# Kernel optimization log

Hardware: AMD Instinct MI355X
Metric: run time of the kernel (lower is better)

## Reference

```python
import jax, jax.numpy as jnp
import numpy as np

B, T = 64, 512
V, E, H, L = 100000, 256, 256, 9


def _lstm(x, Wx, Wh, b):
    # x: [B,T,E] -> hs: [B,T,H]; Keras gate order i,f,c,o
    xg = jnp.einsum('bte,eg->btg', x, Wx) + b  # [B,T,4H]
    h0 = jnp.zeros((x.shape[0], Wh.shape[0]), x.dtype)

    def step(carry, xt):
        h, c = carry
        g = xt + h @ Wh
        i, f, gc, o = jnp.split(g, 4, axis=-1)
        c = jax.nn.sigmoid(f) * c + jax.nn.sigmoid(i) * jnp.tanh(gc)
        h = jax.nn.sigmoid(o) * jnp.tanh(c)
        return (h, c), h

    _, hs = jax.lax.scan(step, (h0, h0), jnp.swapaxes(xg, 0, 1))
    return jnp.swapaxes(hs, 0, 1)


def _crf_log_likelihood(logits, tags, seq_len, trans):
    # logits: [B,T,L], tags: [B,T] int, seq_len: [B] int, trans: [L,L]
    Bb, Tt, Ll = logits.shape
    t_idx = jnp.arange(Tt)
    mask = (t_idx[None, :] < seq_len[:, None]).astype(logits.dtype)  # [B,T]
    # gold path score: unary + pairwise transitions
    unary = jnp.take_along_axis(logits, tags[..., None], axis=-1)[..., 0]  # [B,T]
    unary_score = jnp.sum(unary * mask, axis=-1)
    binary = trans[tags[:, :-1], tags[:, 1:]]  # [B,T-1]
    binary_score = jnp.sum(binary * mask[:, 1:], axis=-1)
    score = unary_score + binary_score
    # forward algorithm (log partition)
    alpha0 = logits[:, 0]  # [B,L]
    step_mask = t_idx[1:, None] < seq_len[None, :]  # [T-1,B]

    def step(alpha, xs):
        logit_t, m = xs  # [B,L], [B]
        new = jax.nn.logsumexp(alpha[:, :, None] + trans[None], axis=1) + logit_t
        alpha = jnp.where(m[:, None], new, alpha)
        return alpha, None

    alpha, _ = jax.lax.scan(step, alpha0, (jnp.swapaxes(logits[:, 1:], 0, 1), step_mask))
    log_norm = jax.nn.logsumexp(alpha, axis=-1)  # [B]
    return score - log_norm


def setup_inputs() -> dict:
    key = jax.random.key(0)
    ks = jax.random.split(key, 12)
    s = 0.05
    return {
        'tokens': jax.random.randint(ks[0], (B, T), 0, V),
        'labels': jax.random.randint(ks[1], (B, T), 0, L),
        'emb_table': jax.random.normal(ks[2], (V, E), jnp.float32) * s,
        'Wx_f': jax.random.normal(ks[3], (E, 4 * H), jnp.float32) * s,
        'Wh_f': jax.random.normal(ks[4], (H, 4 * H), jnp.float32) * s,
        'b_f': jnp.zeros((4 * H,), jnp.float32),
        'Wx_b': jax.random.normal(ks[5], (E, 4 * H), jnp.float32) * s,
        'Wh_b': jax.random.normal(ks[6], (H, 4 * H), jnp.float32) * s,
        'b_b': jnp.zeros((4 * H,), jnp.float32),
        'W_dense': jax.random.normal(ks[7], (2 * H, L), jnp.float32) * s,
        'b_dense': jnp.zeros((L,), jnp.float32),
        'trans': jax.random.uniform(ks[8], (L, L), jnp.float32),
    }


def reference(tokens, labels, emb_table, Wx_f, Wh_f, b_f, Wx_b, Wh_b, b_b, W_dense, b_dense, trans):
    # seq_len = count of non-pad (nonzero) tokens, as in the original call()
    seq_len = jnp.sum((tokens != 0).astype(jnp.int32), axis=-1)  # [B]
    emb = emb_table[tokens]  # [B,T,E]  (dropout inactive at inference)
    h_fwd = _lstm(emb, Wx_f, Wh_f, b_f)
    h_bwd = _lstm(emb[:, ::-1], Wx_b, Wh_b, b_b)[:, ::-1]
    enc = jnp.concatenate([h_fwd, h_bwd], axis=-1)  # [B,T,2H]
    logits = enc @ W_dense + b_dense  # [B,T,L]
    ll = _crf_log_likelihood(logits, labels, seq_len, trans)  # [B]
    return logits, seq_len, ll
```

## Files before the change

### kernel.cpp

```cpp
#include <hip/hip_runtime.h>
#include <hip/hip_fp16.h>


typedef unsigned int  uint32;
typedef unsigned short ushort16;
typedef unsigned long long uint64;
typedef __attribute__((ext_vector_type(8))) short  short8;
typedef __attribute__((ext_vector_type(4))) float  floatx4;
typedef __attribute__((ext_vector_type(2))) _Float16 half2t;

#define BB 64
#define TT 512
#define NT (BB*TT)
#define G4 1024
#define NL 9

__device__ inline float bf2f(ushort16 u) {
  return __builtin_bit_cast(float, ((uint32)u) << 16);
}
__device__ inline ushort16 f2bf(float f) {
  uint32 u = __builtin_bit_cast(uint32, f);
  u += 0x7fffu + ((u >> 16) & 1u);
  return (ushort16)(u >> 16);
}
__device__ inline float sigf(float x)  { return 1.0f / (1.0f + __expf(-x)); }
__device__ inline float tanhf_(float x){ return 1.0f - 2.0f / (1.0f + __expf(2.0f * x)); }

__device__ inline float fdot2_(uint32 w, half2t h, float acc) {
  return __builtin_amdgcn_fdot2(__builtin_bit_cast(half2t, w), h, acc, false);
}

__device__ inline void bar_lds() {
  __builtin_amdgcn_sched_barrier(0);
  asm volatile("s_waitcnt lgkmcnt(0)" ::: "memory");
  __builtin_amdgcn_s_barrier();
  __builtin_amdgcn_sched_barrier(0);
}

__global__ __launch_bounds__(64) void k_seqlen(const int* __restrict__ tokens,
                                               int* __restrict__ slen,
                                               float* __restrict__ out_sl) {
  const int b = blockIdx.x, lane = threadIdx.x;
  int cnt = 0;
  for (int t = lane; t < TT; t += 64) cnt += (tokens[b * TT + t] != 0) ? 1 : 0;
  #pragma unroll
  for (int off = 32; off >= 1; off >>= 1) cnt += __shfl_down(cnt, off, 64);
  if (lane == 0) { slen[b] = cnt; out_sl[b] = (float)cnt; }
}

__global__ __launch_bounds__(256) void k_embed(const int* __restrict__ tokens,
                                               const float* __restrict__ emb,
                                               ushort16* __restrict__ A) {
  const int f = blockIdx.x * 256 + threadIdx.x;
  const int e = f * 4;
  const int row = e >> 8;
  const int col = e & 255;
  const int tok = tokens[row];
  const float4 v = *(const float4*)(emb + (size_t)tok * 256 + col);
  uint32 lo = (uint32)f2bf(v.x) | ((uint32)f2bf(v.y) << 16);
  uint32 hi = (uint32)f2bf(v.z) | ((uint32)f2bf(v.w) << 16);
  *(uint2*)(A + e) = make_uint2(lo, hi);
}

__global__ __launch_bounds__(256) void k_wxprep(const float* __restrict__ Wxf,
                                                const float* __restrict__ Wxb,
                                                ushort16* __restrict__ BT) {
  const int id = blockIdx.x * 256 + threadIdx.x;
  const int c = id >> 8, k = id & 255;
  const float v = (c < G4) ? Wxf[k * G4 + c] : Wxb[k * G4 + (c - G4)];
  BT[c * 256 + k] = f2bf(v);
}

__global__ __launch_bounds__(256) void k_whprep(const float* __restrict__ Wh,
                                                uint32* __restrict__ W2) {
  const int id = blockIdx.x * 256 + threadIdx.x;
  const int k2 = id >> 10, c = id & 1023;
  const float w0 = Wh[(2 * k2) * G4 + c];
  const float w1 = Wh[(2 * k2 + 1) * G4 + c];
  const ushort16 b0 = __builtin_bit_cast(ushort16, (_Float16)w0);
  const ushort16 b1 = __builtin_bit_cast(ushort16, (_Float16)w1);
  W2[id] = ((uint32)b1 << 16) | (uint32)b0;
}

__global__ __launch_bounds__(256) void k_gemm_xg(const ushort16* __restrict__ A,
                                                 const ushort16* __restrict__ BT,
                                                 const float* __restrict__ bias_f,
                                                 const float* __restrict__ bias_b,
                                                 ushort16* __restrict__ xgf,
                                                 ushort16* __restrict__ xgb) {
  __shared__ __align__(16) ushort16 As[64 * 36];
  __shared__ __align__(16) ushort16 Bs[64 * 36];
  const int m0 = blockIdx.x * 64;
  const int n0 = blockIdx.y * 64;
  const int tid = threadIdx.x;
  const int wave = tid >> 6, lane = tid & 63;
  const int lr = tid >> 2;
  const int lc = (tid & 3) * 8;
  const int am = lane & 15, aq = lane >> 4;
  floatx4 acc[4];
  #pragma unroll
  for (int j = 0; j < 4; ++j) acc[j] = (floatx4){0.f, 0.f, 0.f, 0.f};

  for (int k0 = 0; k0 < 256; k0 += 32) {
    const uint4 va = *(const uint4*)(A  + ((m0 + lr) * 256 + k0 + lc));
    const uint4 vb = *(const uint4*)(BT + ((n0 + lr) * 256 + k0 + lc));
    *(uint2*)&As[lr * 36 + lc]     = make_uint2(va.x, va.y);
    *(uint2*)&As[lr * 36 + lc + 4] = make_uint2(va.z, va.w);
    *(uint2*)&Bs[lr * 36 + lc]     = make_uint2(vb.x, vb.y);
    *(uint2*)&Bs[lr * 36 + lc + 4] = make_uint2(vb.z, vb.w);
    __syncthreads();
    union { uint2 u[2]; short8 s; } fa, fb;
    fa.u[0] = *(const uint2*)&As[(wave * 16 + am) * 36 + aq * 8];
    fa.u[1] = *(const uint2*)&As[(wave * 16 + am) * 36 + aq * 8 + 4];
    #pragma unroll
    for (int j = 0; j < 4; ++j) {
      fb.u[0] = *(const uint2*)&Bs[(j * 16 + am) * 36 + aq * 8];
      fb.u[1] = *(const uint2*)&Bs[(j * 16 + am) * 36 + aq * 8 + 4];
      acc[j] = __builtin_amdgcn_mfma_f32_16x16x32_bf16(fa.s, fb.s, acc[j], 0, 0, 0);
    }
    __syncthreads();
  }
  const int orow = m0 + wave * 16 + aq * 4;
  #pragma unroll
  for (int j = 0; j < 4; ++j) {
    const int col = n0 + j * 16 + am;
    const float bv = (col < G4) ? bias_f[col] : bias_b[col - G4];
    #pragma unroll
    for (int r = 0; r < 4; ++r) {
      const float v = acc[j][r] + bv;
      const int row = orow + r;
      if (col < G4) xgf[row * G4 + col] = f2bf(v);
      else          xgb[row * G4 + (col - G4)] = f2bf(v);
    }
  }
}

__global__ __launch_bounds__(256) void k_zero(uint64* __restrict__ xh) {
  xh[blockIdx.x * 256 + threadIdx.x] = 0ull;
}

__global__ __launch_bounds__(512, 2) void k_lstm(const ushort16* __restrict__ xgf,
                                                 const ushort16* __restrict__ xgb,
                                                 const uint32* __restrict__ Whf,
                                                 const uint32* __restrict__ Whb,
                                                 uint64* __restrict__ xh,
                                                 float* __restrict__ enc) {
  __shared__ __align__(16) uint32 h2[2][128];
  __shared__ float gl[512];
  const int bid  = blockIdx.x;
  const int dir  = bid >> 7;
  const int b    = (bid >> 1) & 63;
  const int half = bid & 1;
  const int tid  = threadIdx.x;
  const int l = tid & 63;
  const int q = tid >> 7, r = tid & 127;
  const int col = q * 256 + half * 128 + r;
  const ushort16* __restrict__ xg = dir ? xgb : xgf;
  const uint32* __restrict__ W2   = dir ? Whb : Whf;
  uint64* const xmine = xh + ((size_t)bid << 7);
  const uint64* const xpeer = xh + ((size_t)(bid ^ 1) << 7);

  const int ownBase  = half * 64;
  const int peerBase = 64 - ownBase;
  uint32 wv[128];
  #pragma unroll
  for (int i = 0; i < 64; ++i) wv[i]      = W2[(ownBase  + i) * 1024 + col];
  #pragma unroll
  for (int i = 0; i < 64; ++i) wv[64 + i] = W2[(peerBase + i) * 1024 + col];
  #pragma unroll
  for (int i = 0; i < 128; ++i) asm volatile("" : "+v"(wv[i]));

  if (tid < 128) { h2[0][tid] = 0u; }
  float c_state = 0.f;
  __syncthreads();

  const int t0 = dir ? (TT - 1) : 0;
  ushort16 xA = xg[(size_t)(b * TT + t0) * G4 + col];

#define HC(u) __builtin_bit_cast(half2t, u)
#define GR4(B) { const uint4 hq = hb[B]; \
                 a0 = fdot2_(wv[(B)*4+0], HC(hq.x), a0); \
                 a1 = fdot2_(wv[(B)*4+1], HC(hq.y), a1); \
                 a2 = fdot2_(wv[(B)*4+2], HC(hq.z), a2); \
                 a3 = fdot2_(wv[(B)*4+3], HC(hq.w), a3); }

  for (int s = 0; s < TT; ++s) {
    const int par = s & 1;
    float a0 = bf2f(xA), a1 = 0.f, a2 = 0.f, a3 = 0.f;
    if (s + 1 < TT) {
      const int t1 = dir ? (TT - 2 - s) : (s + 1);
      xA = xg[(size_t)(b * TT + t1) * G4 + col];
    }
    const uint64* ppeer = xpeer + (par << 6) + l;
    uint64 pv_ = 0;
    if (s > 0) {
      pv_ = __hip_atomic_load(ppeer, __ATOMIC_RELAXED, __HIP_MEMORY_SCOPE_AGENT);
    }
    __builtin_amdgcn_sched_barrier(0);
    const uint4* hb = (const uint4*)h2[par];
    GR4(0)  GR4(1)  GR4(2)  GR4(3)  GR4(4)  GR4(5)  GR4(6)  GR4(7)
    GR4(8)  GR4(9)  GR4(10) GR4(11) GR4(12) GR4(13) GR4(14) GR4(15)
    if (s > 0) {
      const uint32 want = (uint32)s;
      while (!__all((uint32)(pv_ >> 32) == want)) {
        __builtin_amdgcn_s_sleep(1);
        pv_ = __hip_atomic_load(ppeer, __ATOMIC_RELAXED, __HIP_MEMORY_SCOPE_AGENT);
      }
      h2[par][64 + l] = (uint32)pv_;
    }
    __builtin_amdgcn_sched_barrier(0);
    asm volatile("s_waitcnt lgkmcnt(0)" ::: "memory");
    __builtin_amdgcn_sched_barrier(0);
    GR4(16) GR4(17) GR4(18) GR4(19) GR4(20) GR4(21) GR4(22) GR4(23)
    GR4(24) GR4(25) GR4(26) GR4(27) GR4(28) GR4(29) GR4(30) GR4(31)
    {
      float tv = (a0 + a1) + (a2 + a3);
      tv = (q == 2) ? tanhf_(tv) : sigf(tv);
      gl[tid] = tv;
    }
    bar_lds();
    if (tid < 128) {
      const float I = gl[tid];
      const float F = gl[128 + tid];
      const float G = gl[256 + tid];
      const float O = gl[384 + tid];
      c_state = F * c_state + I * G;
      const float h = O * tanhf_(c_state);
      const int hv = (int)(uint32)__builtin_bit_cast(ushort16, (_Float16)h);
      const int ho = __shfl_xor(hv, 1, 64);
      if (!(tid & 1)) {
        const uint32 pk = ((uint32)hv & 0xffffu) | ((uint32)ho << 16);
        if (s + 1 < TT) {
          const uint64 pv = ((uint64)(uint32)(s + 1) << 32) | (uint64)pk;
          __hip_atomic_store(xmine + ((par ^ 1) << 6) + (tid >> 1), pv,
                             __ATOMIC_RELAXED, __HIP_MEMORY_SCOPE_AGENT);
        }
        h2[par ^ 1][tid >> 1] = pk;
      }
      const int t = dir ? (TT - 1 - s) : s;
      enc[(size_t)(b * TT + t) * 512 + dir * 256 + half * 128 + tid] = h;
    }
    bar_lds();
  }
#undef HC
#undef GR4
}

__global__ __launch_bounds__(256) void k_dense(const float* __restrict__ enc,
                                               const float* __restrict__ Wd,
                                               const float* __restrict__ bd,
                                               float* __restrict__ logits) {
  __shared__ float Wl[512 * NL];
  __shared__ float bl[NL];
  const int tid = threadIdx.x;
  for (int i = tid; i < 512 * NL; i += 256) Wl[i] = Wd[i];
  if (tid < NL) bl[tid] = bd[tid];
  __syncthreads();
  const int wave = tid >> 6, lane = tid & 63;
  const int row = blockIdx.x * 4 + wave;
  const float* er = enc + (size_t)row * 512;
  float p[NL];
  #pragma unroll
  for (int c = 0; c < NL; ++c) p[c] = 0.f;
  #pragma unroll
  for (int u = 0; u < 8; ++u) {
    const int k = u * 64 + lane;
    const float v = er[k];
    const float* wr = &Wl[k * NL];
    #pragma unroll
    for (int c = 0; c < NL; ++c) p[c] += v * wr[c];
  }
  #pragma unroll
  for (int c = 0; c < NL; ++c) {
    #pragma unroll
    for (int off = 32; off >= 1; off >>= 1) p[c] += __shfl_down(p[c], off, 64);
  }
  if (lane == 0) {
    float* orow = logits + (size_t)row * NL;
    #pragma unroll
    for (int c = 0; c < NL; ++c) orow[c] = p[c] + bl[c];
  }
}

__global__ __launch_bounds__(64) void k_crf(const float* __restrict__ logits,
                                            const int* __restrict__ labels,
                                            const int* __restrict__ slen,
                                            const float* __restrict__ trans,
                                            float* __restrict__ out_ll) {
  __shared__ float tr[NL * NL];
  __shared__ float alpha[NL];
  const int b = blockIdx.x;
  const int lane = threadIdx.x;
  for (int i = lane; i < NL * NL; i += 64) tr[i] = trans[i];
  __syncthreads();
  const int len = slen[b];
  const int* tg = labels + b * TT;
  const float* lg = logits + (size_t)b * TT * NL;
  float s = 0.f;
  for (int t = lane; t < TT; t += 64)
    if (t < len) s += lg[t * NL + tg[t]];
  for (int t = lane; t < TT - 1; t += 64)
    if (t + 1 < len) s += tr[tg[t] * NL + tg[t + 1]];
  #pragma unroll
  for (int off = 32; off >= 1; off >>= 1) s += __shfl_down(s, off, 64);
  if (lane < NL) alpha[lane] = lg[lane];
  __syncthreads();
  if (lane < NL) {
    const int j = lane;
    for (int t = 1; t < TT; ++t) {
      if (t < len) {
        float av[NL];
        float m = -1e30f;
        #pragma unroll
        for (int i = 0; i < NL; ++i) { av[i] = alpha[i] + tr[i * NL + j]; m = fmaxf(m, av[i]); }
        float ss = 0.f;
        #pragma unroll
        for (int i = 0; i < NL; ++i) ss += __expf(av[i] - m);
        const float nj = m + __logf(ss) + lg[t * NL + j];
        alpha[j] = nj;
      }
    }
  }
  __syncthreads();
  if (lane == 0) {
    float m = -1e30f;
    #pragma unroll
    for (int i = 0; i < NL; ++i) m = fmaxf(m, alpha[i]);
    float ss = 0.f;
    #pragma unroll
    for (int i = 0; i < NL; ++i) ss += __expf(alpha[i] - m);
    out_ll[b] = s - (m + __logf(ss));
  }
}

extern "C" void kernel_launch(void* const* d_in, const int* in_sizes, int n_in,
                              void* d_out, int out_size, void* d_ws, size_t ws_size,
                              hipStream_t stream) {
  (void)in_sizes; (void)n_in; (void)out_size; (void)ws_size;
  const int*   tokens = (const int*)d_in[0];
  const int*   labels = (const int*)d_in[1];
  const float* emb    = (const float*)d_in[2];
  const float* Wxf    = (const float*)d_in[3];
  const float* Whf    = (const float*)d_in[4];
  const float* bf_    = (const float*)d_in[5];
  const float* Wxb    = (const float*)d_in[6];
  const float* Whb    = (const float*)d_in[7];
  const float* bb_    = (const float*)d_in[8];
  const float* Wd     = (const float*)d_in[9];
  const float* bd     = (const float*)d_in[10];
  const float* trans  = (const float*)d_in[11];
  float* out = (float*)d_out;

  char* ws = (char*)d_ws;
  ushort16* A    = (ushort16*)(ws + 0);
  ushort16* BT   = (ushort16*)(ws + 16777216);
  uint32*   W2f  = (uint32*)  (ws + 17825792);
  uint32*   W2b  = (uint32*)  (ws + 18350080);
  ushort16* xgf  = (ushort16*)(ws + 18874368);
  ushort16* xgb  = (ushort16*)(ws + 85983232);
  float*    enc  = (float*)   (ws + 153092096);
  int*      slen = (int*)     (ws + 220200960);
  uint64*   xh   = (uint64*)  (ws + 0);

  k_seqlen<<<BB, 64, 0, stream>>>(tokens, slen, out + NT * NL);
  k_embed <<<NT * 256 / 4 / 256, 256, 0, stream>>>(tokens, emb, A);
  k_wxprep<<<2048 * 256 / 256, 256, 0, stream>>>(Wxf, Wxb, BT);
  k_whprep<<<128 * 1024 / 256, 256, 0, stream>>>(Whf, W2f);
  k_whprep<<<128 * 1024 / 256, 256, 0, stream>>>(Whb, W2b);
  k_gemm_xg<<<dim3(NT / 64, 2048 / 64), 256, 0, stream>>>(A, BT, bf_, bb_, xgf, xgb);
  k_zero  <<<128, 256, 0, stream>>>(xh);
  k_lstm  <<<256, 512, 0, stream>>>(xgf, xgb, W2f, W2b, xh, enc);
  k_dense <<<NT / 4, 256, 0, stream>>>(enc, Wd, bd, out);
  k_crf   <<<BB, 64, 0, stream>>>(out, labels, slen, trans, out + NT * NL + BB);
}
```

Before: 1.329 ms.

## Process two batch rows per LSTM block to overlap peer exchange waits

```diff
diff --git a/kernel.cpp b/kernel.cpp
--- a/kernel.cpp
+++ b/kernel.cpp
@@ -146,19 +146,20 @@
                                                  uint64* __restrict__ xh,
                                                  float* __restrict__ enc) {
   __shared__ __align__(16) uint32 h2[2][128];
-  __shared__ float gl[512];
+  __shared__ float gl[2][512];
   const int bid  = blockIdx.x;
-  const int dir  = bid >> 7;
-  const int b    = (bid >> 1) & 63;
+  const int dir  = bid >> 6;
+  const int pp   = (bid >> 1) & 31;
   const int half = bid & 1;
+  const int b0   = pp, b1 = pp + 32;
   const int tid  = threadIdx.x;
   const int l = tid & 63;
   const int q = tid >> 7, r = tid & 127;
   const int col = q * 256 + half * 128 + r;
   const ushort16* __restrict__ xg = dir ? xgb : xgf;
   const uint32* __restrict__ W2   = dir ? Whb : Whf;
-  uint64* const xmine = xh + ((size_t)bid << 7);
-  const uint64* const xpeer = xh + ((size_t)(bid ^ 1) << 7);
+  uint64* const xmine = xh + ((size_t)bid << 8);
+  const uint64* const xpeer = xh + ((size_t)(bid ^ 1) << 8);
 
   const int ownBase  = half * 64;
   const int peerBase = 64 - ownBase;
@@ -170,80 +171,111 @@
   #pragma unroll
   for (int i = 0; i < 128; ++i) asm volatile("" : "+v"(wv[i]));
 
-  if (tid < 128) { h2[0][tid] = 0u; }
+  if (tid < 256) h2[tid >> 7][tid & 127] = 0u;
   float c_state = 0.f;
   __syncthreads();
 
   const int t0 = dir ? (TT - 1) : 0;
-  ushort16 xA = xg[(size_t)(b * TT + t0) * G4 + col];
+  ushort16 xA0 = xg[(size_t)(b0 * TT + t0) * G4 + col];
+  ushort16 xA1 = xg[(size_t)(b1 * TT + t0) * G4 + col];
 
 #define HC(u) __builtin_bit_cast(half2t, u)
-#define GR4(B) { const uint4 hq = hb[B]; \
-                 a0 = fdot2_(wv[(B)*4+0], HC(hq.x), a0); \
-                 a1 = fdot2_(wv[(B)*4+1], HC(hq.y), a1); \
-                 a2 = fdot2_(wv[(B)*4+2], HC(hq.z), a2); \
-                 a3 = fdot2_(wv[(B)*4+3], HC(hq.w), a3); }
+#define GR4(HB,B,A0,A1,A2,A3) { const uint4 hq = (HB)[B]; \
+                 A0 = fdot2_(wv[(B)*4+0], HC(hq.x), A0); \
+                 A1 = fdot2_(wv[(B)*4+1], HC(hq.y), A1); \
+                 A2 = fdot2_(wv[(B)*4+2], HC(hq.z), A2); \
+                 A3 = fdot2_(wv[(B)*4+3], HC(hq.w), A3); }
+#define PH16(HB,S,A0,A1,A2,A3) \
+  GR4(HB,(S)+0,A0,A1,A2,A3)  GR4(HB,(S)+1,A0,A1,A2,A3)  GR4(HB,(S)+2,A0,A1,A2,A3)  GR4(HB,(S)+3,A0,A1,A2,A3) \
+  GR4(HB,(S)+4,A0,A1,A2,A3)  GR4(HB,(S)+5,A0,A1,A2,A3)  GR4(HB,(S)+6,A0,A1,A2,A3)  GR4(HB,(S)+7,A0,A1,A2,A3) \
+  GR4(HB,(S)+8,A0,A1,A2,A3)  GR4(HB,(S)+9,A0,A1,A2,A3)  GR4(HB,(S)+10,A0,A1,A2,A3) GR4(HB,(S)+11,A0,A1,A2,A3) \
+  GR4(HB,(S)+12,A0,A1,A2,A3) GR4(HB,(S)+13,A0,A1,A2,A3) GR4(HB,(S)+14,A0,A1,A2,A3) GR4(HB,(S)+15,A0,A1,A2,A3)
 
   for (int s = 0; s < TT; ++s) {
     const int par = s & 1;
-    float a0 = bf2f(xA), a1 = 0.f, a2 = 0.f, a3 = 0.f;
+    float a0 = bf2f(xA0), a1 = 0.f, a2 = 0.f, a3 = 0.f;
+    float e0 = bf2f(xA1), e1 = 0.f, e2 = 0.f, e3 = 0.f;
     if (s + 1 < TT) {
       const int t1 = dir ? (TT - 2 - s) : (s + 1);
-      xA = xg[(size_t)(b * TT + t1) * G4 + col];
-    }
-    const uint64* ppeer = xpeer + (par << 6) + l;
-    uint64 pv_ = 0;
+      xA0 = xg[(size_t)(b0 * TT + t1) * G4 + col];
+      xA1 = xg[(size_t)(b1 * TT + t1) * G4 + col];
+    }
+    const uint64* ppeer0 = xpeer +       (par << 6) + l;
+    const uint64* ppeer1 = xpeer + 128 + (par << 6) + l;
+    uint64 pv0 = 0, pv1 = 0;
     if (s > 0) {
-      pv_ = __hip_atomic_load(ppeer, __ATOMIC_RELAXED, __HIP_MEMORY_SCOPE_AGENT);
+      pv0 = __hip_atomic_load(ppeer0, __ATOMIC_RELAXED, __HIP_MEMORY_SCOPE_AGENT);
+      pv1 = __hip_atomic_load(ppeer1, __ATOMIC_RELAXED, __HIP_MEMORY_SCOPE_AGENT);
     }
     __builtin_amdgcn_sched_barrier(0);
-    const uint4* hb = (const uint4*)h2[par];
-    GR4(0)  GR4(1)  GR4(2)  GR4(3)  GR4(4)  GR4(5)  GR4(6)  GR4(7)
-    GR4(8)  GR4(9)  GR4(10) GR4(11) GR4(12) GR4(13) GR4(14) GR4(15)
+    const uint4* hb0 = (const uint4*)h2[0];
+    const uint4* hb1 = (const uint4*)h2[1];
+    PH16(hb0, 0, a0, a1, a2, a3)
+    PH16(hb1, 0, e0, e1, e2, e3)
     if (s > 0) {
       const uint32 want = (uint32)s;
-      while (!__all((uint32)(pv_ >> 32) == want)) {
+      while (!__all((uint32)(pv0 >> 32) == want)) {
         __builtin_amdgcn_s_sleep(1);
-        pv_ = __hip_atomic_load(ppeer, __ATOMIC_RELAXED, __HIP_MEMORY_SCOPE_AGENT);
+        pv0 = __hip_atomic_load(ppeer0, __ATOMIC_RELAXED, __HIP_MEMORY_SCOPE_AGENT);
       }
-      h2[par][64 + l] = (uint32)pv_;
+      h2[0][64 + l] = (uint32)pv0;
     }
     __builtin_amdgcn_sched_barrier(0);
     asm volatile("s_waitcnt lgkmcnt(0)" ::: "memory");
     __builtin_amdgcn_sched_barrier(0);
-    GR4(16) GR4(17) GR4(18) GR4(19) GR4(20) GR4(21) GR4(22) GR4(23)
-    GR4(24) GR4(25) GR4(26) GR4(27) GR4(28) GR4(29) GR4(30) GR4(31)
+    PH16(hb0, 16, a0, a1, a2, a3)
     {
       float tv = (a0 + a1) + (a2 + a3);
       tv = (q == 2) ? tanhf_(tv) : sigf(tv);
-      gl[tid] = tv;
+      gl[0][tid] = tv;
+    }
+    if (s > 0) {
+      const uint32 want = (uint32)s;
+      while (!__all((uint32)(pv1 >> 32) == want)) {
+        __builtin_amdgcn_s_sleep(1);
+        pv1 = __hip_atomic_load(ppeer1, __ATOMIC_RELAXED, __HIP_MEMORY_SCOPE_AGENT);
+      }
+      h2[1][64 + l] = (uint32)pv1;
+    }
+    __builtin_amdgcn_sched_barrier(0);
+    asm volatile("s_waitcnt lgkmcnt(0)" ::: "memory");
+    __builtin_amdgcn_sched_barrier(0);
+    PH16(hb1, 16, e0, e1, e2, e3)
+    {
+      float tv = (e0 + e1) + (e2 + e3);
+      tv = (q == 2) ? tanhf_(tv) : sigf(tv);
+      gl[1][tid] = tv;
     }
     bar_lds();
-    if (tid < 128) {
-      const float I = gl[tid];
-      const float F = gl[128 + tid];
-      const float G = gl[256 + tid];
-      const float O = gl[384 + tid];
+    if (tid < 256) {
+      const int js = tid >> 7;
+      const int u  = tid & 127;
+      const float I = gl[js][u];
+      const float F = gl[js][128 + u];
+      const float G = gl[js][256 + u];
+      const float O = gl[js][384 + u];
       c_state = F * c_state + I * G;
       const float h = O * tanhf_(c_state);
       const int hv = (int)(uint32)__builtin_bit_cast(ushort16, (_Float16)h);
       const int ho = __shfl_xor(hv, 1, 64);
-      if (!(tid & 1)) {
+      if (!(u & 1)) {
         const uint32 pk = ((uint32)hv & 0xffffu) | ((uint32)ho << 16);
         if (s + 1 < TT) {
           const uint64 pv = ((uint64)(uint32)(s + 1) << 32) | (uint64)pk;
-          __hip_atomic_store(xmine + ((par ^ 1) << 6) + (tid >> 1), pv,
+          __hip_atomic_store(xmine + (js << 7) + ((par ^ 1) << 6) + (u >> 1), pv,
                              __ATOMIC_RELAXED, __HIP_MEMORY_SCOPE_AGENT);
         }
-        h2[par ^ 1][tid >> 1] = pk;
+        h2[js][u >> 1] = pk;
       }
       const int t = dir ? (TT - 1 - s) : s;
-      enc[(size_t)(b * TT + t) * 512 + dir * 256 + half * 128 + tid] = h;
+      const int b = js ? b1 : b0;
+      enc[(size_t)(b * TT + t) * 512 + dir * 256 + half * 128 + u] = h;
     }
     bar_lds();
   }
 #undef HC
 #undef GR4
+#undef PH16
 }
 
 __global__ __launch_bounds__(256) void k_dense(const float* __restrict__ enc,
@@ -369,7 +401,7 @@
   k_whprep<<<128 * 1024 / 256, 256, 0, stream>>>(Whb, W2b);
   k_gemm_xg<<<dim3(NT / 64, 2048 / 64), 256, 0, stream>>>(A, BT, bf_, bb_, xgf, xgb);
   k_zero  <<<128, 256, 0, stream>>>(xh);
-  k_lstm  <<<256, 512, 0, stream>>>(xgf, xgb, W2f, W2b, xh, enc);
+  k_lstm  <<<128, 512, 0, stream>>>(xgf, xgb, W2f, W2b, xh, enc);
   k_dense <<<NT / 4, 256, 0, stream>>>(enc, Wd, bd, out);
   k_crf   <<<BB, 64, 0, stream>>>(out, labels, slen, trans, out + NT * NL + BB);
 }
```

After: 2.827 ms. 2.13x slower.

## Split LSTM recurrent dot product across two thread groups per gate column

Applied to the files above, without the earlier changes.

```diff
diff --git a/kernel.cpp b/kernel.cpp
--- a/kernel.cpp
+++ b/kernel.cpp
@@ -139,84 +139,93 @@
   xh[blockIdx.x * 256 + threadIdx.x] = 0ull;
 }
 
-__global__ __launch_bounds__(512, 2) void k_lstm(const ushort16* __restrict__ xgf,
-                                                 const ushort16* __restrict__ xgb,
-                                                 const uint32* __restrict__ Whf,
-                                                 const uint32* __restrict__ Whb,
-                                                 uint64* __restrict__ xh,
-                                                 float* __restrict__ enc) {
+__global__ __launch_bounds__(1024, 1) void k_lstm(const ushort16* __restrict__ xgf,
+                                                  const ushort16* __restrict__ xgb,
+                                                  const uint32* __restrict__ Whf,
+                                                  const uint32* __restrict__ Whb,
+                                                  uint64* __restrict__ xh,
+                                                  float* __restrict__ enc) {
   __shared__ __align__(16) uint32 h2[2][128];
   __shared__ float gl[512];
+  __shared__ float glp[512];
   const int bid  = blockIdx.x;
   const int dir  = bid >> 7;
   const int b    = (bid >> 1) & 63;
   const int half = bid & 1;
   const int tid  = threadIdx.x;
-  const int l = tid & 63;
-  const int q = tid >> 7, r = tid & 127;
+  const int l    = tid & 63;
+  const int c512 = tid & 511;
+  const int q = c512 >> 7, r = c512 & 127;
   const int col = q * 256 + half * 128 + r;
+  const bool ownk = (tid < 512);
   const ushort16* __restrict__ xg = dir ? xgb : xgf;
   const uint32* __restrict__ W2   = dir ? Whb : Whf;
   uint64* const xmine = xh + ((size_t)bid << 7);
   const uint64* const xpeer = xh + ((size_t)(bid ^ 1) << 7);
 
-  const int ownBase  = half * 64;
-  const int peerBase = 64 - ownBase;
-  uint32 wv[128];
-  #pragma unroll
-  for (int i = 0; i < 64; ++i) wv[i]      = W2[(ownBase  + i) * 1024 + col];
-  #pragma unroll
-  for (int i = 0; i < 64; ++i) wv[64 + i] = W2[(peerBase + i) * 1024 + col];
-  #pragma unroll
-  for (int i = 0; i < 128; ++i) asm volatile("" : "+v"(wv[i]));
-
-  if (tid < 128) { h2[0][tid] = 0u; }
+  const int rowbase = ownk ? (half * 64) : (64 - half * 64);
+  uint32 wv[64];
+  #pragma unroll
+  for (int i = 0; i < 64; ++i) wv[i] = W2[(rowbase + i) * 1024 + col];
+  #pragma unroll
+  for (int i = 0; i < 64; ++i) asm volatile("" : "+v"(wv[i]));
+
+  if (tid < 128) h2[0][tid] = 0u;
   float c_state = 0.f;
   __syncthreads();
 
-  const int t0 = dir ? (TT - 1) : 0;
-  ushort16 xA = xg[(size_t)(b * TT + t0) * G4 + col];
+  ushort16 xA = (ushort16)0;
+  if (ownk) {
+    const int t0 = dir ? (TT - 1) : 0;
+    xA = xg[(size_t)(b * TT + t0) * G4 + col];
+  }
 
 #define HC(u) __builtin_bit_cast(half2t, u)
-#define GR4(B) { const uint4 hq = hb[B]; \
-                 a0 = fdot2_(wv[(B)*4+0], HC(hq.x), a0); \
-                 a1 = fdot2_(wv[(B)*4+1], HC(hq.y), a1); \
-                 a2 = fdot2_(wv[(B)*4+2], HC(hq.z), a2); \
-                 a3 = fdot2_(wv[(B)*4+3], HC(hq.w), a3); }
+#define GR4(B,W) { const uint4 hq = hb[B]; \
+                 a0 = fdot2_(wv[(W)*4+0], HC(hq.x), a0); \
+                 a1 = fdot2_(wv[(W)*4+1], HC(hq.y), a1); \
+                 a2 = fdot2_(wv[(W)*4+2], HC(hq.z), a2); \
+                 a3 = fdot2_(wv[(W)*4+3], HC(hq.w), a3); }
 
   for (int s = 0; s < TT; ++s) {
     const int par = s & 1;
-    float a0 = bf2f(xA), a1 = 0.f, a2 = 0.f, a3 = 0.f;
-    if (s + 1 < TT) {
-      const int t1 = dir ? (TT - 2 - s) : (s + 1);
-      xA = xg[(size_t)(b * TT + t1) * G4 + col];
-    }
-    const uint64* ppeer = xpeer + (par << 6) + l;
-    uint64 pv_ = 0;
-    if (s > 0) {
-      pv_ = __hip_atomic_load(ppeer, __ATOMIC_RELAXED, __HIP_MEMORY_SCOPE_AGENT);
-    }
-    __builtin_amdgcn_sched_barrier(0);
+    float a0 = 0.f, a1 = 0.f, a2 = 0.f, a3 = 0.f;
     const uint4* hb = (const uint4*)h2[par];
-    GR4(0)  GR4(1)  GR4(2)  GR4(3)  GR4(4)  GR4(5)  GR4(6)  GR4(7)
-    GR4(8)  GR4(9)  GR4(10) GR4(11) GR4(12) GR4(13) GR4(14) GR4(15)
-    if (s > 0) {
-      const uint32 want = (uint32)s;
-      while (!__all((uint32)(pv_ >> 32) == want)) {
-        __builtin_amdgcn_s_sleep(1);
-        pv_ = __hip_atomic_load(ppeer, __ATOMIC_RELAXED, __HIP_MEMORY_SCOPE_AGENT);
+    if (ownk) {
+      a0 = bf2f(xA);
+      if (s + 1 < TT) {
+        const int t1 = dir ? (TT - 2 - s) : (s + 1);
+        xA = xg[(size_t)(b * TT + t1) * G4 + col];
       }
-      h2[par][64 + l] = (uint32)pv_;
-    }
-    __builtin_amdgcn_sched_barrier(0);
-    asm volatile("s_waitcnt lgkmcnt(0)" ::: "memory");
-    __builtin_amdgcn_sched_barrier(0);
-    GR4(16) GR4(17) GR4(18) GR4(19) GR4(20) GR4(21) GR4(22) GR4(23)
-    GR4(24) GR4(25) GR4(26) GR4(27) GR4(28) GR4(29) GR4(30) GR4(31)
-    {
-      float tv = (a0 + a1) + (a2 + a3);
-      tv = (q == 2) ? tanhf_(tv) : sigf(tv);
-      gl[tid] = tv;
+      GR4(0,0)   GR4(1,1)   GR4(2,2)   GR4(3,3)
+      GR4(4,4)   GR4(5,5)   GR4(6,6)   GR4(7,7)
+      GR4(8,8)   GR4(9,9)   GR4(10,10) GR4(11,11)
+      GR4(12,12) GR4(13,13) GR4(14,14) GR4(15,15)
+    } else {
+      if (s > 0) {
+        const uint64* pp = xpeer + (par << 6) + l;
+        const uint32 want = (uint32)s;
+        uint64 pv = __hip_atomic_load(pp, __ATOMIC_RELAXED, __HIP_MEMORY_SCOPE_AGENT);
+        while (!__all((uint32)(pv >> 32) == want)) {
+          __builtin_amdgcn_s_sleep(1);
+          pv = __hip_atomic_load(pp, __ATOMIC_RELAXED, __HIP_MEMORY_SCOPE_AGENT);
+        }
+        h2[par][64 + l] = (uint32)pv;
+        __builtin_amdgcn_sched_barrier(0);
+        asm volatile("s_waitcnt lgkmcnt(0)" ::: "memory");
+        __builtin_amdgcn_sched_barrier(0);
+      }
+      GR4(16,0)  GR4(17,1)  GR4(18,2)  GR4(19,3)
+      GR4(20,4)  GR4(21,5)  GR4(22,6)  GR4(23,7)
+      GR4(24,8)  GR4(25,9)  GR4(26,10) GR4(27,11)
+      GR4(28,12) GR4(29,13) GR4(30,14) GR4(31,15)
+      glp[c512] = (a0 + a1) + (a2 + a3);
+    }
+    bar_lds();
+    if (ownk) {
+      float v = ((a0 + a1) + (a2 + a3)) + glp[c512];
+      v = (q == 2) ? tanhf_(v) : sigf(v);
+      gl[c512] = v;
     }
     bar_lds();
     if (tid < 128) {
@@ -369,7 +378,7 @@
   k_whprep<<<128 * 1024 / 256, 256, 0, stream>>>(Whb, W2b);
   k_gemm_xg<<<dim3(NT / 64, 2048 / 64), 256, 0, stream>>>(A, BT, bf_, bb_, xgf, xgb);
   k_zero  <<<128, 256, 0, stream>>>(xh);
-  k_lstm  <<<256, 512, 0, stream>>>(xgf, xgb, W2f, W2b, xh, enc);
+  k_lstm  <<<256, 1024, 0, stream>>>(xgf, xgb, W2f, W2b, xh, enc);
   k_dense <<<NT / 4, 256, 0, stream>>>(enc, Wd, bd, out);
   k_crf   <<<BB, 64, 0, stream>>>(out, labels, slen, trans, out + NT * NL + BB);
 }
```

Result: faster. 1.243 ms (-6.5%).
